# Kernel optimization log

Measured on AMD Instinct MI355X. Metric: run time of the kernel, lower is better.

## Reference

```python
import jax, jax.numpy as jnp
import numpy as np

B, S, D = 2, 2048, 1024
H = 2048          # expert hidden size; up-proj width is 2*H (GLU)
E = 8             # num_experts
K = 2             # top_k


def setup_inputs() -> dict:
    key = jax.random.key(0)
    k1, k2, k3, k4, k5 = jax.random.split(key, 5)
    x = jax.random.normal(k1, (B, S, D), dtype=jnp.float32)
    expert_p = jax.random.uniform(k2, (B, S, K), dtype=jnp.float32)
    expert_idxs = jax.random.randint(k3, (B, S, K), 0, E)
    W1 = jax.random.normal(k4, (E, D, 2 * H), dtype=jnp.float32) * 0.02
    W2 = jax.random.normal(k5, (E, H, D), dtype=jnp.float32) * 0.02
    return {"x": x, "expert_p": expert_p, "expert_idxs": expert_idxs, "W1": W1, "W2": W2}


def reference(x, expert_p, expert_idxs, W1, W2):
    # x: [B, S, D]; expert_p/expert_idxs: [B, S, K]; W1: [E, D, 2H]; W2: [E, H, D]
    x_shape = x.shape
    d = x_shape[-1]
    k = expert_idxs.shape[-1]
    n_experts = W1.shape[0]
    xf = x.reshape(-1, d)                      # [T, D]
    T = xf.shape[0]
    e_flat = expert_idxs.reshape(-1)           # [P] token-major pair order, P = T*k
    xp = jnp.repeat(xf, k, axis=0)             # [P, D] matches e_flat ordering

    # Grouped up-projection: each (token, expert) pair hits its expert's W1.
    up = jnp.zeros((T * k, W1.shape[-1]), dtype=x.dtype)
    for e in range(n_experts):                 # fixed small loop over experts
        up = up + jnp.where((e_flat == e)[:, None], xp @ W1[e], 0)

    # Fused GLU: chunk(2), exact GELU (torch nn.GELU default), gate (g + 1).
    h, g = jnp.split(up, 2, axis=-1)           # [P, H] each
    a = jax.nn.gelu(h, approximate=False) * (g + 1)

    # Grouped down-projection.
    down = jnp.zeros((T * k, d), dtype=x.dtype)
    for e in range(n_experts):
        down = down + jnp.where((e_flat == e)[:, None], a @ W2[e], 0)

    # Gated scatter-combine over the top_k pairs of each token.
    gates = expert_p.reshape(T, k)             # [T, K]
    y = jnp.sum(down.reshape(T, k, d) * gates[..., None], axis=1)
    return y.reshape(*x_shape[:-1], d)
```

## Files before the change

kernel.cpp:

```cpp
#include <hip/hip_runtime.h>
#include <hip/hip_bf16.h>
#include <math.h>

#define TT 4096
#define PP 8192
#define DD 1024
#define HH 2048
#define EE 8
#define CC1 4096

typedef __attribute__((ext_vector_type(8))) short s16x8;
typedef __attribute__((ext_vector_type(4))) float f32x4;

#define W1T_OFF   0ull
#define W2T_OFF   (W1T_OFF + (size_t)EE*DD*CC1*2)
#define XB_OFF    (W2T_OFF + (size_t)EE*HH*DD*2)
#define ABUF_OFF  (XB_OFF  + (size_t)TT*DD*2)
#define DOWN_OFF  (ABUF_OFF + (size_t)PP*HH*2)
#define META_OFF  (DOWN_OFF + (size_t)PP*DD*4)
#define PAIR_OFF  (META_OFF + 2048)
#define POS_OFF   (PAIR_OFF + (size_t)PP*4)

#define VMCNT(N) asm volatile("s_waitcnt vmcnt(" #N ")" ::: "memory")
#define CFENCE() asm volatile("" ::: "memory")

__device__ __forceinline__ unsigned short f2bf(float f) {
  union { float f; unsigned u; } a; a.f = f;
  unsigned u = a.u;
  unsigned r = u + 0x7FFFu + ((u >> 16) & 1u);
  return (unsigned short)(r >> 16);
}

__device__ __forceinline__ void gload16(const void* g, void* l) {
  __builtin_amdgcn_global_load_lds(
      (const __attribute__((address_space(1))) void*)(uintptr_t)g,
      (__attribute__((address_space(3))) void*)(unsigned)(uintptr_t)l,
      16, 0, 0);
}

__global__ void k_cvt_x(const float* __restrict__ in, unsigned short* __restrict__ out, int n4) {
  int i = blockIdx.x * blockDim.x + threadIdx.x;
  if (i >= n4) return;
  float4 v = reinterpret_cast<const float4*>(in)[i];
  ushort4 o;
  o.x = f2bf(v.x); o.y = f2bf(v.y); o.z = f2bf(v.z); o.w = f2bf(v.w);
  reinterpret_cast<ushort4*>(out)[i] = o;
}

__global__ __launch_bounds__(256) void k_transpose(const float* __restrict__ in,
                                                   unsigned short* __restrict__ out,
                                                   int R, int C) {
  __shared__ float t[64][65];
  const size_t mbase = (size_t)blockIdx.z * (size_t)R * (size_t)C;
  int c0 = blockIdx.x * 64, r0 = blockIdx.y * 64;
  int tid = threadIdx.x;
#pragma unroll
  for (int i = 0; i < 4; ++i) {
    int ch = tid + i * 256;
    int row = ch >> 4, c4 = (ch & 15) * 4;
    float4 v = *reinterpret_cast<const float4*>(&in[mbase + (size_t)(r0 + row) * C + c0 + c4]);
    t[row][c4] = v.x; t[row][c4 + 1] = v.y; t[row][c4 + 2] = v.z; t[row][c4 + 3] = v.w;
  }
  __syncthreads();
#pragma unroll
  for (int i = 0; i < 4; ++i) {
    int ch = tid + i * 256;
    int c = ch >> 4, rb = (ch & 15) * 4;
    ushort4 o;
    o.x = f2bf(t[rb][c]); o.y = f2bf(t[rb + 1][c]);
    o.z = f2bf(t[rb + 2][c]); o.w = f2bf(t[rb + 3][c]);
    *reinterpret_cast<ushort4*>(&out[mbase + (size_t)(c0 + c) * R + r0 + rb]) = o;
  }
}

__global__ void k_route(const int* __restrict__ eidx, int* __restrict__ meta,
                        int* __restrict__ plist, int* __restrict__ pos) {
  __shared__ int cnt[EE], off[EE + 1], cur[EE];
  int tid = threadIdx.x;
  if (tid < EE) { cnt[tid] = 0; cur[tid] = 0; }
  __syncthreads();
  for (int p = tid; p < PP; p += blockDim.x) atomicAdd(&cnt[eidx[p]], 1);
  __syncthreads();
  if (tid == 0) {
    int s = 0;
    for (int e = 0; e < EE; ++e) { off[e] = s; s += cnt[e]; }
    off[EE] = s;
    int n256 = 0;
    for (int e = 0; e < EE; ++e)
      for (int r = 0; r < cnt[e]; r += 256) {
        meta[16 + 2*n256] = e; meta[17 + 2*n256] = off[e] + r; ++n256;
      }
    meta[0] = n256;
    for (int e = 0; e <= EE; ++e) meta[1 + e] = off[e];
  }
  __syncthreads();
  for (int p = tid; p < PP; p += blockDim.x) {
    int e = eidx[p];
    int q = off[e] + atomicAdd(&cur[e], 1);
    plist[q] = p;
    pos[p] = q;
  }
}

__global__ __launch_bounds__(512) void k_gemm1(
    const unsigned short* __restrict__ xb,
    const unsigned short* __restrict__ w1t,
    const float* __restrict__ gates,
    const int* __restrict__ meta,
    const int* __restrict__ plist,
    unsigned short* __restrict__ abuf)
{
  const int nt = meta[0];
  const int tb = blockIdx.x;
  if (tb >= nt) return;
  const int e  = meta[16 + 2*tb];
  const int q0 = meta[17 + 2*tb];
  const int nrows = min(256, meta[2 + e] - q0);
  const int c0 = blockIdx.y * 64;

  __shared__ unsigned short As[3][256 * 64];
  __shared__ unsigned short Bs[3][128 * 64];

  const int tid = threadIdx.x;
  const int wave = tid >> 6, lane = tid & 63;
  const int l15 = lane & 15, l4 = lane >> 4;
  const int wr = wave >> 1, wc = wave & 1;

  const unsigned short* w1e = w1t + (size_t)e * CC1 * DD;

  const unsigned short* aga[4];
  const unsigned short* bga[2];
#pragma unroll
  for (int i = 0; i < 4; ++i) {
    int c = tid + i * 512;
    int row = c >> 3;
    int ko = ((c & 7) ^ (row & 7)) * 8;
    int r = row < nrows ? row : 0;
    int p = plist[q0 + r];
    aga[i] = xb + (size_t)(p >> 1) * DD + ko;
  }
#pragma unroll
  for (int i = 0; i < 2; ++i) {
    int c = tid + i * 512;
    int row = c >> 3;
    int ko = ((c & 7) ^ (row & 7)) * 8;
    int u = row & 63, wcq = row >> 6;
    int col = (u < 32) ? (c0 + wcq * 32 + u) : (HH + c0 + wcq * 32 + (u - 32));
    bga[i] = w1e + (size_t)col * DD + ko;
  }

  f32x4 acc[4][4];
#pragma unroll
  for (int a = 0; a < 4; ++a)
#pragma unroll
    for (int b = 0; b < 4; ++b) acc[a][b] = (f32x4)0.0f;

  auto stage = [&](int kk, unsigned short* pa, unsigned short* pb) {
#pragma unroll
    for (int i = 0; i < 4; ++i) gload16(aga[i] + kk, pa + (tid + i * 512) * 8);
#pragma unroll
    for (int i = 0; i < 2; ++i) gload16(bga[i] + kk, pb + (tid + i * 512) * 8);
  };

  auto compute_tile = [&](const unsigned short* sa, const unsigned short* sb) {
    const char* A8 = (const char*)sa;
    const char* B8 = (const char*)sb;
#pragma unroll
    for (int ks = 0; ks < 2; ++ks) {
      s16x8 af[4], bfr[4];
#pragma unroll
      for (int rf = 0; rf < 4; ++rf) {
        int row = wr * 64 + rf * 16 + l15;
        af[rf] = *(const s16x8*)(A8 + ((row * 128 + ks * 64 + l4 * 16) ^ ((row & 7) << 4)));
      }
#pragma unroll
      for (int cf = 0; cf < 4; ++cf) {
        int row = wc * 64 + cf * 16 + l15;
        bfr[cf] = *(const s16x8*)(B8 + ((row * 128 + ks * 64 + l4 * 16) ^ ((row & 7) << 4)));
      }
      __builtin_amdgcn_s_setprio(1);
#pragma unroll
      for (int rf = 0; rf < 4; ++rf)
#pragma unroll
        for (int cf = 0; cf < 4; ++cf)
          acc[rf][cf] = __builtin_amdgcn_mfma_f32_16x16x32_bf16(af[rf], bfr[cf], acc[rf][cf], 0, 0, 0);
      __builtin_amdgcn_s_setprio(0);
    }
  };

  unsigned short *a0 = As[0], *a1 = As[1], *a2 = As[2];
  unsigned short *b0 = Bs[0], *b1 = Bs[1], *b2 = Bs[2];

  stage(0, a0, b0);
  stage(64, a1, b1);
  VMCNT(6);
  __builtin_amdgcn_s_barrier();
  CFENCE();

  for (int kt = 0; kt < DD / 64 - 2; ++kt) {
    stage((kt + 2) * 64, a2, b2);
    compute_tile(a0, b0);
    VMCNT(6);
    __builtin_amdgcn_s_barrier();
    CFENCE();
    unsigned short* t;
    t = a0; a0 = a1; a1 = a2; a2 = t;
    t = b0; b0 = b1; b1 = b2; b2 = t;
  }
  compute_tile(a0, b0);
  VMCNT(0);
  __builtin_amdgcn_s_barrier();
  CFENCE();
  compute_tile(a1, b1);

#pragma unroll
  for (int rf = 0; rf < 4; ++rf) {
#pragma unroll
    for (int i = 0; i < 4; ++i) {
      int r = wr * 64 + rf * 16 + l4 * 4 + i;
      if (r < nrows) {
        int q = q0 + r;
        float gt = gates[plist[q]];
        unsigned short* orow = abuf + (size_t)q * HH + c0 + wc * 32 + l15;
#pragma unroll
        for (int cf = 0; cf < 2; ++cf) {
          float hv = acc[rf][cf][i];
          float gv = acc[rf][cf + 2][i];
          float av = 0.5f * hv * (1.0f + erff(hv * 0.70710678118654752f)) * (gv + 1.0f) * gt;
          orow[cf * 16] = f2bf(av);
        }
      }
    }
  }
}

__global__ __launch_bounds__(512) void k_gemm2(
    const unsigned short* __restrict__ abuf,
    const unsigned short* __restrict__ w2t,
    const int* __restrict__ meta,
    float* __restrict__ down)
{
  const int nt = meta[0];
  const int tb = blockIdx.x;
  if (tb >= nt) return;
  const int e  = meta[16 + 2*tb];
  const int q0 = meta[17 + 2*tb];
  const int nrows = min(256, meta[2 + e] - q0);
  const int c0 = blockIdx.y * 128;

  __shared__ unsigned short As[3][256 * 64];
  __shared__ unsigned short Bs[3][128 * 64];

  const int tid = threadIdx.x;
  const int wave = tid >> 6, lane = tid & 63;
  const int l15 = lane & 15, l4 = lane >> 4;
  const int wr = wave >> 1, wc = wave & 1;

  const unsigned short* w2e = w2t + (size_t)e * DD * HH;

  const unsigned short* aga[4];
  const unsigned short* bga[2];
#pragma unroll
  for (int i = 0; i < 4; ++i) {
    int c = tid + i * 512;
    int row = c >> 3;
    int ko = ((c & 7) ^ (row & 7)) * 8;
    int r = row < nrows ? row : 0;
    aga[i] = abuf + (size_t)(q0 + r) * HH + ko;
  }
#pragma unroll
  for (int i = 0; i < 2; ++i) {
    int c = tid + i * 512;
    int row = c >> 3;
    int ko = ((c & 7) ^ (row & 7)) * 8;
    bga[i] = w2e + (size_t)(c0 + row) * HH + ko;
  }

  f32x4 acc[4][4];
#pragma unroll
  for (int a = 0; a < 4; ++a)
#pragma unroll
    for (int b = 0; b < 4; ++b) acc[a][b] = (f32x4)0.0f;

  auto stage = [&](int kk, unsigned short* pa, unsigned short* pb) {
#pragma unroll
    for (int i = 0; i < 4; ++i) gload16(aga[i] + kk, pa + (tid + i * 512) * 8);
#pragma unroll
    for (int i = 0; i < 2; ++i) gload16(bga[i] + kk, pb + (tid + i * 512) * 8);
  };

  auto compute_tile = [&](const unsigned short* sa, const unsigned short* sb) {
    const char* A8 = (const char*)sa;
    const char* B8 = (const char*)sb;
#pragma unroll
    for (int ks = 0; ks < 2; ++ks) {
      s16x8 af[4], bfr[4];
#pragma unroll
      for (int rf = 0; rf < 4; ++rf) {
        int row = wr * 64 + rf * 16 + l15;
        af[rf] = *(const s16x8*)(A8 + ((row * 128 + ks * 64 + l4 * 16) ^ ((row & 7) << 4)));
      }
#pragma unroll
      for (int cf = 0; cf < 4; ++cf) {
        int row = wc * 64 + cf * 16 + l15;
        bfr[cf] = *(const s16x8*)(B8 + ((row * 128 + ks * 64 + l4 * 16) ^ ((row & 7) << 4)));
      }
      __builtin_amdgcn_s_setprio(1);
#pragma unroll
      for (int rf = 0; rf < 4; ++rf)
#pragma unroll
        for (int cf = 0; cf < 4; ++cf)
          acc[rf][cf] = __builtin_amdgcn_mfma_f32_16x16x32_bf16(af[rf], bfr[cf], acc[rf][cf], 0, 0, 0);
      __builtin_amdgcn_s_setprio(0);
    }
  };

  unsigned short *a0 = As[0], *a1 = As[1], *a2 = As[2];
  unsigned short *b0 = Bs[0], *b1 = Bs[1], *b2 = Bs[2];

  stage(0, a0, b0);
  stage(64, a1, b1);
  VMCNT(6);
  __builtin_amdgcn_s_barrier();
  CFENCE();

  for (int kt = 0; kt < HH / 64 - 2; ++kt) {
    stage((kt + 2) * 64, a2, b2);
    compute_tile(a0, b0);
    VMCNT(6);
    __builtin_amdgcn_s_barrier();
    CFENCE();
    unsigned short* t;
    t = a0; a0 = a1; a1 = a2; a2 = t;
    t = b0; b0 = b1; b1 = b2; b2 = t;
  }
  compute_tile(a0, b0);
  VMCNT(0);
  __builtin_amdgcn_s_barrier();
  CFENCE();
  compute_tile(a1, b1);

#pragma unroll
  for (int rf = 0; rf < 4; ++rf) {
#pragma unroll
    for (int i = 0; i < 4; ++i) {
      int r = wr * 64 + rf * 16 + l4 * 4 + i;
      if (r < nrows) {
        int q = q0 + r;
        float* orow = down + (size_t)q * DD + c0 + wc * 64 + l15;
#pragma unroll
        for (int cf = 0; cf < 4; ++cf) orow[cf * 16] = acc[rf][cf][i];
      }
    }
  }
}

__global__ void k_combine(const float* __restrict__ down, const int* __restrict__ pos,
                          float* __restrict__ y) {
  int i = blockIdx.x * blockDim.x + threadIdx.x;
  if (i >= TT * DD / 4) return;
  int t = i >> 8;
  int c4 = i & 255;
  int qa = pos[2 * t], qb = pos[2 * t + 1];
  float4 a = reinterpret_cast<const float4*>(down + (size_t)qa * DD)[c4];
  float4 b = reinterpret_cast<const float4*>(down + (size_t)qb * DD)[c4];
  float4 o; o.x = a.x + b.x; o.y = a.y + b.y; o.z = a.z + b.z; o.w = a.w + b.w;
  reinterpret_cast<float4*>(y)[i] = o;
}

extern "C" void kernel_launch(void* const* d_in, const int* in_sizes, int n_in,
                              void* d_out, int out_size, void* d_ws, size_t ws_size,
                              hipStream_t stream) {
  const float* x  = (const float*)d_in[0];
  const float* ep = (const float*)d_in[1];
  const int*   ei = (const int*)d_in[2];
  const float* W1 = (const float*)d_in[3];
  const float* W2 = (const float*)d_in[4];
  float* y = (float*)d_out;
  char* ws = (char*)d_ws;

  unsigned short* w1t = (unsigned short*)(ws + W1T_OFF);
  unsigned short* w2t = (unsigned short*)(ws + W2T_OFF);
  unsigned short* xb  = (unsigned short*)(ws + XB_OFF);
  unsigned short* ab  = (unsigned short*)(ws + ABUF_OFF);
  float* down = (float*)(ws + DOWN_OFF);
  int* meta   = (int*)(ws + META_OFF);
  int* plist  = (int*)(ws + PAIR_OFF);
  int* pos    = (int*)(ws + POS_OFF);

  hipLaunchKernelGGL(k_cvt_x, dim3(TT * DD / 4 / 256), dim3(256), 0, stream,
                     x, xb, TT * DD / 4);
  hipLaunchKernelGGL(k_transpose, dim3(CC1 / 64, DD / 64, EE), dim3(256), 0, stream,
                     W1, w1t, DD, CC1);
  hipLaunchKernelGGL(k_transpose, dim3(DD / 64, HH / 64, EE), dim3(256), 0, stream,
                     W2, w2t, HH, DD);
  hipLaunchKernelGGL(k_route, dim3(1), dim3(256), 0, stream, ei, meta, plist, pos);
  hipLaunchKernelGGL(k_gemm1, dim3(40, 32), dim3(512), 0, stream,
                     xb, w1t, ep, meta, plist, ab);
  hipLaunchKernelGGL(k_gemm2, dim3(40, 8), dim3(512), 0, stream,
                     ab, w2t, meta, down);
  hipLaunchKernelGGL(k_combine, dim3(TT * DD / 4 / 256), dim3(256), 0, stream,
                     down, pos, y);
}
```

Before: 285.6 us.

## Retile up-projection GEMM to 256x256 tiles with 4-stage K=32 pipeline

```diff
diff --git a/kernel.cpp b/kernel.cpp
--- a/kernel.cpp
+++ b/kernel.cpp
@@ -102,7 +102,7 @@
   }
 }
 
-__global__ __launch_bounds__(512) void k_gemm1(
+__global__ __launch_bounds__(512, 2) void k_gemm1(
     const unsigned short* __restrict__ xb,
     const unsigned short* __restrict__ w1t,
     const float* __restrict__ gates,
@@ -116,118 +116,107 @@
   const int e  = meta[16 + 2*tb];
   const int q0 = meta[17 + 2*tb];
   const int nrows = min(256, meta[2 + e] - q0);
-  const int c0 = blockIdx.y * 64;
-
-  __shared__ unsigned short As[3][256 * 64];
-  __shared__ unsigned short Bs[3][128 * 64];
+  const int c0 = blockIdx.y * 128;
+
+  __shared__ unsigned short As[4][256 * 32];
+  __shared__ unsigned short Bs[4][256 * 32];
 
   const int tid = threadIdx.x;
   const int wave = tid >> 6, lane = tid & 63;
   const int l15 = lane & 15, l4 = lane >> 4;
-  const int wr = wave >> 1, wc = wave & 1;
+  const int wm = wave >> 2, wn = wave & 3;
 
   const unsigned short* w1e = w1t + (size_t)e * CC1 * DD;
 
-  const unsigned short* aga[4];
+  const unsigned short* aga[2];
   const unsigned short* bga[2];
 #pragma unroll
-  for (int i = 0; i < 4; ++i) {
+  for (int i = 0; i < 2; ++i) {
     int c = tid + i * 512;
-    int row = c >> 3;
-    int ko = ((c & 7) ^ (row & 7)) * 8;
+    int row = c >> 2;
+    int kc = c & 3;
+    int ko = (kc ^ (row & 3)) * 8;
     int r = row < nrows ? row : 0;
     int p = plist[q0 + r];
     aga[i] = xb + (size_t)(p >> 1) * DD + ko;
-  }
-#pragma unroll
-  for (int i = 0; i < 2; ++i) {
-    int c = tid + i * 512;
-    int row = c >> 3;
-    int ko = ((c & 7) ^ (row & 7)) * 8;
-    int u = row & 63, wcq = row >> 6;
-    int col = (u < 32) ? (c0 + wcq * 32 + u) : (HH + c0 + wcq * 32 + (u - 32));
+    int b = row >> 4, u = row & 15;
+    int col = ((b & 1) ? HH : 0) + c0 + (b >> 1) * 16 + u;
     bga[i] = w1e + (size_t)col * DD + ko;
   }
 
-  f32x4 acc[4][4];
-#pragma unroll
-  for (int a = 0; a < 4; ++a)
+  f32x4 acc[8][4];
+#pragma unroll
+  for (int a = 0; a < 8; ++a)
 #pragma unroll
     for (int b = 0; b < 4; ++b) acc[a][b] = (f32x4)0.0f;
 
-  auto stage = [&](int kk, unsigned short* pa, unsigned short* pb) {
-#pragma unroll
-    for (int i = 0; i < 4; ++i) gload16(aga[i] + kk, pa + (tid + i * 512) * 8);
+  const int swz = (l4 ^ (l15 & 3)) << 4;
+
+  auto stage = [&](int u) {
+    unsigned short* pa = As[u & 3];
+    unsigned short* pb = Bs[u & 3];
+    const int kk = u * 32;
+#pragma unroll
+    for (int i = 0; i < 2; ++i) gload16(aga[i] + kk, pa + (tid + i * 512) * 8);
 #pragma unroll
     for (int i = 0; i < 2; ++i) gload16(bga[i] + kk, pb + (tid + i * 512) * 8);
   };
 
-  auto compute_tile = [&](const unsigned short* sa, const unsigned short* sb) {
-    const char* A8 = (const char*)sa;
-    const char* B8 = (const char*)sb;
-#pragma unroll
-    for (int ks = 0; ks < 2; ++ks) {
-      s16x8 af[4], bfr[4];
-#pragma unroll
-      for (int rf = 0; rf < 4; ++rf) {
-        int row = wr * 64 + rf * 16 + l15;
-        af[rf] = *(const s16x8*)(A8 + ((row * 128 + ks * 64 + l4 * 16) ^ ((row & 7) << 4)));
-      }
-#pragma unroll
-      for (int cf = 0; cf < 4; ++cf) {
-        int row = wc * 64 + cf * 16 + l15;
-        bfr[cf] = *(const s16x8*)(B8 + ((row * 128 + ks * 64 + l4 * 16) ^ ((row & 7) << 4)));
-      }
-      __builtin_amdgcn_s_setprio(1);
-#pragma unroll
-      for (int rf = 0; rf < 4; ++rf)
-#pragma unroll
-        for (int cf = 0; cf < 4; ++cf)
-          acc[rf][cf] = __builtin_amdgcn_mfma_f32_16x16x32_bf16(af[rf], bfr[cf], acc[rf][cf], 0, 0, 0);
-      __builtin_amdgcn_s_setprio(0);
-    }
+  auto phase = [&](int u, bool dostage) {
+    const char* A8 = (const char*)As[u & 3];
+    const char* B8 = (const char*)Bs[u & 3];
+    s16x8 af[8], bfr[4];
+#pragma unroll
+    for (int rf = 0; rf < 8; ++rf) {
+      int row = wm * 128 + rf * 16 + l15;
+      af[rf] = *(const s16x8*)(A8 + row * 64 + swz);
+    }
+#pragma unroll
+    for (int cf = 0; cf < 4; ++cf) {
+      int brow = wn * 64 + cf * 16 + l15;
+      bfr[cf] = *(const s16x8*)(B8 + brow * 64 + swz);
+    }
+    if (dostage) stage(u + 3);
+    __builtin_amdgcn_s_setprio(1);
+#pragma unroll
+    for (int rf = 0; rf < 8; ++rf)
+#pragma unroll
+      for (int cf = 0; cf < 4; ++cf)
+        acc[rf][cf] = __builtin_amdgcn_mfma_f32_16x16x32_bf16(af[rf], bfr[cf], acc[rf][cf], 0, 0, 0);
+    __builtin_amdgcn_s_setprio(0);
   };
 
-  unsigned short *a0 = As[0], *a1 = As[1], *a2 = As[2];
-  unsigned short *b0 = Bs[0], *b1 = Bs[1], *b2 = Bs[2];
-
-  stage(0, a0, b0);
-  stage(64, a1, b1);
-  VMCNT(6);
-  __builtin_amdgcn_s_barrier();
-  CFENCE();
-
-  for (int kt = 0; kt < DD / 64 - 2; ++kt) {
-    stage((kt + 2) * 64, a2, b2);
-    compute_tile(a0, b0);
-    VMCNT(6);
+  const int NU = DD / 32;
+
+  stage(0); stage(1); stage(2);
+  for (int u = 0; u < NU - 3; ++u) {
+    VMCNT(8);
     __builtin_amdgcn_s_barrier();
     CFENCE();
-    unsigned short* t;
-    t = a0; a0 = a1; a1 = a2; a2 = t;
-    t = b0; b0 = b1; b1 = b2; b2 = t;
-  }
-  compute_tile(a0, b0);
-  VMCNT(0);
-  __builtin_amdgcn_s_barrier();
-  CFENCE();
-  compute_tile(a1, b1);
-
-#pragma unroll
-  for (int rf = 0; rf < 4; ++rf) {
+    phase(u, true);
+  }
+  VMCNT(8); __builtin_amdgcn_s_barrier(); CFENCE();
+  phase(NU - 3, false);
+  VMCNT(4); __builtin_amdgcn_s_barrier(); CFENCE();
+  phase(NU - 2, false);
+  VMCNT(0); __builtin_amdgcn_s_barrier(); CFENCE();
+  phase(NU - 1, false);
+
+#pragma unroll
+  for (int rf = 0; rf < 8; ++rf) {
 #pragma unroll
     for (int i = 0; i < 4; ++i) {
-      int r = wr * 64 + rf * 16 + l4 * 4 + i;
+      int r = wm * 128 + rf * 16 + l4 * 4 + i;
       if (r < nrows) {
         int q = q0 + r;
         float gt = gates[plist[q]];
-        unsigned short* orow = abuf + (size_t)q * HH + c0 + wc * 32 + l15;
-#pragma unroll
-        for (int cf = 0; cf < 2; ++cf) {
-          float hv = acc[rf][cf][i];
-          float gv = acc[rf][cf + 2][i];
+        unsigned short* orow = abuf + (size_t)q * HH + c0 + wn * 32 + l15;
+#pragma unroll
+        for (int j = 0; j < 2; ++j) {
+          float hv = acc[rf][2 * j][i];
+          float gv = acc[rf][2 * j + 1][i];
           float av = 0.5f * hv * (1.0f + erff(hv * 0.70710678118654752f)) * (gv + 1.0f) * gt;
-          orow[cf * 16] = f2bf(av);
+          orow[j * 16] = f2bf(av);
         }
       }
     }
@@ -305,13 +294,11 @@
         int row = wc * 64 + cf * 16 + l15;
         bfr[cf] = *(const s16x8*)(B8 + ((row * 128 + ks * 64 + l4 * 16) ^ ((row & 7) << 4)));
       }
-      __builtin_amdgcn_s_setprio(1);
 #pragma unroll
       for (int rf = 0; rf < 4; ++rf)
 #pragma unroll
         for (int cf = 0; cf < 4; ++cf)
           acc[rf][cf] = __builtin_amdgcn_mfma_f32_16x16x32_bf16(af[rf], bfr[cf], acc[rf][cf], 0, 0, 0);
-      __builtin_amdgcn_s_setprio(0);
     }
   };
 
@@ -395,7 +382,7 @@
   hipLaunchKernelGGL(k_transpose, dim3(DD / 64, HH / 64, EE), dim3(256), 0, stream,
                      W2, w2t, HH, DD);
   hipLaunchKernelGGL(k_route, dim3(1), dim3(256), 0, stream, ei, meta, plist, pos);
-  hipLaunchKernelGGL(k_gemm1, dim3(40, 32), dim3(512), 0, stream,
+  hipLaunchKernelGGL(k_gemm1, dim3(40, 16), dim3(512), 0, stream,
                      xb, w1t, ep, meta, plist, ab);
   hipLaunchKernelGGL(k_gemm2, dim3(40, 8), dim3(512), 0, stream,
                      ab, w2t, meta, down);
```

After: 283.8 us. No clear change (-0.6%).

## Split-K the down-projection GEMM into two halves with bf16 partials

Applied to the files above, without the earlier changes.

```diff
diff --git a/kernel.cpp b/kernel.cpp
--- a/kernel.cpp
+++ b/kernel.cpp
@@ -17,7 +17,7 @@
 #define XB_OFF    (W2T_OFF + (size_t)EE*HH*DD*2)
 #define ABUF_OFF  (XB_OFF  + (size_t)TT*DD*2)
 #define DOWN_OFF  (ABUF_OFF + (size_t)PP*HH*2)
-#define META_OFF  (DOWN_OFF + (size_t)PP*DD*4)
+#define META_OFF  (DOWN_OFF + (size_t)2*PP*DD*2)
 #define PAIR_OFF  (META_OFF + 2048)
 #define POS_OFF   (PAIR_OFF + (size_t)PP*4)
 
@@ -29,6 +29,11 @@
   unsigned u = a.u;
   unsigned r = u + 0x7FFFu + ((u >> 16) & 1u);
   return (unsigned short)(r >> 16);
+}
+
+__device__ __forceinline__ float bf2f(unsigned short s) {
+  union { unsigned u; float f; } a; a.u = ((unsigned)s) << 16;
+  return a.f;
 }
 
 __device__ __forceinline__ void gload16(const void* g, void* l) {
@@ -178,13 +183,11 @@
         int row = wc * 64 + cf * 16 + l15;
         bfr[cf] = *(const s16x8*)(B8 + ((row * 128 + ks * 64 + l4 * 16) ^ ((row & 7) << 4)));
       }
-      __builtin_amdgcn_s_setprio(1);
 #pragma unroll
       for (int rf = 0; rf < 4; ++rf)
 #pragma unroll
         for (int cf = 0; cf < 4; ++cf)
           acc[rf][cf] = __builtin_amdgcn_mfma_f32_16x16x32_bf16(af[rf], bfr[cf], acc[rf][cf], 0, 0, 0);
-      __builtin_amdgcn_s_setprio(0);
     }
   };
 
@@ -238,7 +241,7 @@
     const unsigned short* __restrict__ abuf,
     const unsigned short* __restrict__ w2t,
     const int* __restrict__ meta,
-    float* __restrict__ down)
+    unsigned short* __restrict__ down)
 {
   const int nt = meta[0];
   const int tb = blockIdx.x;
@@ -247,6 +250,7 @@
   const int q0 = meta[17 + 2*tb];
   const int nrows = min(256, meta[2 + e] - q0);
   const int c0 = blockIdx.y * 128;
+  const int kz = blockIdx.z * (HH / 2);
 
   __shared__ unsigned short As[3][256 * 64];
   __shared__ unsigned short Bs[3][128 * 64];
@@ -266,14 +270,14 @@
     int row = c >> 3;
     int ko = ((c & 7) ^ (row & 7)) * 8;
     int r = row < nrows ? row : 0;
-    aga[i] = abuf + (size_t)(q0 + r) * HH + ko;
+    aga[i] = abuf + (size_t)(q0 + r) * HH + kz + ko;
   }
 #pragma unroll
   for (int i = 0; i < 2; ++i) {
     int c = tid + i * 512;
     int row = c >> 3;
     int ko = ((c & 7) ^ (row & 7)) * 8;
-    bga[i] = w2e + (size_t)(c0 + row) * HH + ko;
+    bga[i] = w2e + (size_t)(c0 + row) * HH + kz + ko;
   }
 
   f32x4 acc[4][4];
@@ -305,13 +309,11 @@
         int row = wc * 64 + cf * 16 + l15;
         bfr[cf] = *(const s16x8*)(B8 + ((row * 128 + ks * 64 + l4 * 16) ^ ((row & 7) << 4)));
       }
-      __builtin_amdgcn_s_setprio(1);
 #pragma unroll
       for (int rf = 0; rf < 4; ++rf)
 #pragma unroll
         for (int cf = 0; cf < 4; ++cf)
           acc[rf][cf] = __builtin_amdgcn_mfma_f32_16x16x32_bf16(af[rf], bfr[cf], acc[rf][cf], 0, 0, 0);
-      __builtin_amdgcn_s_setprio(0);
     }
   };
 
@@ -324,7 +326,8 @@
   __builtin_amdgcn_s_barrier();
   CFENCE();
 
-  for (int kt = 0; kt < HH / 64 - 2; ++kt) {
+  const int NT = (HH / 2) / 64;
+  for (int kt = 0; kt < NT - 2; ++kt) {
     stage((kt + 2) * 64, a2, b2);
     compute_tile(a0, b0);
     VMCNT(6);
@@ -340,6 +343,7 @@
   CFENCE();
   compute_tile(a1, b1);
 
+  unsigned short* dz = down + (size_t)blockIdx.z * PP * DD;
 #pragma unroll
   for (int rf = 0; rf < 4; ++rf) {
 #pragma unroll
@@ -347,25 +351,35 @@
       int r = wr * 64 + rf * 16 + l4 * 4 + i;
       if (r < nrows) {
         int q = q0 + r;
-        float* orow = down + (size_t)q * DD + c0 + wc * 64 + l15;
-#pragma unroll
-        for (int cf = 0; cf < 4; ++cf) orow[cf * 16] = acc[rf][cf][i];
+        unsigned short* orow = dz + (size_t)q * DD + c0 + wc * 64 + l15;
+#pragma unroll
+        for (int cf = 0; cf < 4; ++cf) orow[cf * 16] = f2bf(acc[rf][cf][i]);
       }
     }
   }
 }
 
-__global__ void k_combine(const float* __restrict__ down, const int* __restrict__ pos,
+__global__ void k_combine(const unsigned short* __restrict__ down, const int* __restrict__ pos,
                           float* __restrict__ y) {
   int i = blockIdx.x * blockDim.x + threadIdx.x;
-  if (i >= TT * DD / 4) return;
-  int t = i >> 8;
-  int c4 = i & 255;
+  if (i >= TT * DD / 8) return;
+  int t = i >> 7;
+  int c8 = (i & 127) * 8;
   int qa = pos[2 * t], qb = pos[2 * t + 1];
-  float4 a = reinterpret_cast<const float4*>(down + (size_t)qa * DD)[c4];
-  float4 b = reinterpret_cast<const float4*>(down + (size_t)qb * DD)[c4];
-  float4 o; o.x = a.x + b.x; o.y = a.y + b.y; o.z = a.z + b.z; o.w = a.w + b.w;
-  reinterpret_cast<float4*>(y)[i] = o;
+  const unsigned short* d0 = down;
+  const unsigned short* d1 = down + (size_t)PP * DD;
+  s16x8 va0 = *reinterpret_cast<const s16x8*>(d0 + (size_t)qa * DD + c8);
+  s16x8 va1 = *reinterpret_cast<const s16x8*>(d1 + (size_t)qa * DD + c8);
+  s16x8 vb0 = *reinterpret_cast<const s16x8*>(d0 + (size_t)qb * DD + c8);
+  s16x8 vb1 = *reinterpret_cast<const s16x8*>(d1 + (size_t)qb * DD + c8);
+  float o[8];
+#pragma unroll
+  for (int j = 0; j < 8; ++j)
+    o[j] = bf2f((unsigned short)va0[j]) + bf2f((unsigned short)va1[j]) +
+           bf2f((unsigned short)vb0[j]) + bf2f((unsigned short)vb1[j]);
+  float4* yo = reinterpret_cast<float4*>(y + (size_t)t * DD + c8);
+  yo[0] = (float4){o[0], o[1], o[2], o[3]};
+  yo[1] = (float4){o[4], o[5], o[6], o[7]};
 }
 
 extern "C" void kernel_launch(void* const* d_in, const int* in_sizes, int n_in,
@@ -383,7 +397,7 @@
   unsigned short* w2t = (unsigned short*)(ws + W2T_OFF);
   unsigned short* xb  = (unsigned short*)(ws + XB_OFF);
   unsigned short* ab  = (unsigned short*)(ws + ABUF_OFF);
-  float* down = (float*)(ws + DOWN_OFF);
+  unsigned short* down = (unsigned short*)(ws + DOWN_OFF);
   int* meta   = (int*)(ws + META_OFF);
   int* plist  = (int*)(ws + PAIR_OFF);
   int* pos    = (int*)(ws + POS_OFF);
@@ -397,8 +411,8 @@
   hipLaunchKernelGGL(k_route, dim3(1), dim3(256), 0, stream, ei, meta, plist, pos);
   hipLaunchKernelGGL(k_gemm1, dim3(40, 32), dim3(512), 0, stream,
                      xb, w1t, ep, meta, plist, ab);
-  hipLaunchKernelGGL(k_gemm2, dim3(40, 8), dim3(512), 0, stream,
+  hipLaunchKernelGGL(k_gemm2, dim3(40, 8, 2), dim3(512), 0, stream,
                      ab, w2t, meta, down);
-  hipLaunchKernelGGL(k_combine, dim3(TT * DD / 4 / 256), dim3(256), 0, stream,
+  hipLaunchKernelGGL(k_combine, dim3(TT * DD / 8 / 256), dim3(256), 0, stream,
                      down, pos, y);
 }
```

New measurement: 270.1 us. 5.4% less time.
